# Kernel optimization log

Measured on AMD Instinct MI355X. Metric: run time of the kernel, lower is better.

The kernel has to match this reference:

```python
import jax, jax.numpy as jnp
import numpy as np

GROUP = 16  # FP4 quantization group size along the K (channel) axis
FP4_MAX = 6.0  # max magnitude representable in e2m1


def _round_e2m1(v):
    """Round to nearest value on the signed e2m1 grid {0,.5,1,1.5,2,3,4,6}."""
    s = jnp.sign(v)
    a = jnp.clip(jnp.abs(v), 0.0, FP4_MAX)
    q = jnp.where(a < 0.25, 0.0,
        jnp.where(a < 0.75, 0.5,
        jnp.where(a < 1.25, 1.0,
        jnp.where(a < 1.75, 1.5,
        jnp.where(a < 2.5, 2.0,
        jnp.where(a < 3.5, 3.0,
        jnp.where(a < 5.0, 4.0, 6.0)))))))
    return s * q


def fake_quant_fp4(x):
    """NVFP4-style fake quantization: per-16 group fp8_e4m3 scale + e2m1 values.

    x: [..., K] with K % 16 == 0. Returns dequantized tensor, same shape/dtype.
    """
    shp = x.shape
    g = x.reshape(shp[:-1] + (shp[-1] // GROUP, GROUP))
    amax = jnp.max(jnp.abs(g), axis=-1, keepdims=True)
    # scale stored as fp8_e4m3 (matches oscales dtype float8_e4m3fn in source)
    scale = (amax / FP4_MAX).astype(jnp.float8_e4m3fn).astype(x.dtype)
    safe = jnp.where(scale > 0, scale, jnp.ones_like(scale))
    q = _round_e2m1(g / safe)
    dq = jnp.where(scale > 0, q * scale, jnp.zeros_like(q))
    return dq.reshape(shp)


def setup_inputs() -> dict:
    key = jax.random.key(0)
    k1, k2, k3 = jax.random.split(key, 3)
    M, K, N = 8192, 4096, 4096
    x = jax.random.normal(k1, (M, K), dtype=jnp.float32)
    weight = jax.random.normal(k2, (N, K), dtype=jnp.float32) * 0.02
    bias = jax.random.normal(k3, (N,), dtype=jnp.float32) * 0.01
    return {"x": x, "weight": weight, "bias": bias}


def reference(x, weight, bias):
    # quantize_input: per-group FP4 fake-quant of activations (smooth == ones)
    xq = fake_quant_fp4(x)
    # __init__ quantizes weight_pad with the same kernel -> qweight/wscales
    wq = fake_quant_fp4(weight)
    # gemm_w4a4 with inline dequant + bias add
    out = jnp.einsum("mk,nk->mn", xq, wq) + bias
    return out
```

## Files before the change

### kernel.cpp

```cpp
#include <hip/hip_runtime.h>
#include <cstdint>


typedef __attribute__((ext_vector_type(8))) __bf16 bf16x8;
typedef __attribute__((ext_vector_type(4))) float f32x4;

typedef __attribute__((address_space(1))) void gvoid;
typedef __attribute__((address_space(3))) void lvoid;

__device__ __forceinline__ float fp8_e4m3_rt(float x) {
    if (x < 0.015625f) {
        return __builtin_rintf(x * 512.0f) * (1.0f / 512.0f);
    }
    unsigned u = __float_as_uint(x);
    unsigned lsb = (u >> 20) & 1u;
    u = (u + 0x7FFFFu + lsb) & ~0xFFFFFu;
    return __uint_as_float(u);
}

__device__ __forceinline__ float round_e2m1(float v) {
    float a = fabsf(v);
    a = fminf(a, 6.0f);
    float q = a < 0.25f ? 0.0f :
              a < 0.75f ? 0.5f :
              a < 1.25f ? 1.0f :
              a < 1.75f ? 1.5f :
              a < 2.5f  ? 2.0f :
              a < 3.5f  ? 3.0f :
              a < 5.0f  ? 4.0f : 6.0f;
    return copysignf(q, v);
}

__global__ __launch_bounds__(256) void quant_fp4(const float* __restrict__ in,
                                                 uint16_t* __restrict__ out,
                                                 int nquads) {
    int i = blockIdx.x * 256 + threadIdx.x;
    if (i >= nquads) return;
    float4 v = ((const float4*)in)[i];
    float a = fmaxf(fmaxf(fabsf(v.x), fabsf(v.y)), fmaxf(fabsf(v.z), fabsf(v.w)));
    a = fmaxf(a, __shfl_xor(a, 1));
    a = fmaxf(a, __shfl_xor(a, 2));
    float scale = fp8_e4m3_rt(a / 6.0f);
    float safe = scale > 0.0f ? scale : 1.0f;
    float vals[4] = {v.x, v.y, v.z, v.w};
    unsigned r[4];
    #pragma unroll
    for (int e = 0; e < 4; ++e) {
        float q = round_e2m1(vals[e] / safe);
        float dq = scale > 0.0f ? q * scale : 0.0f;
        r[e] = __float_as_uint(dq) >> 16;
    }
    uint2 o;
    o.x = r[0] | (r[1] << 16);
    o.y = r[2] | (r[3] << 16);
    ((uint2*)out)[i] = o;
}

#define BM 256
#define BN 256
#define BK 64
#define THREADS 512

__device__ __forceinline__ void barfence() {
    asm volatile("" ::: "memory");
    __builtin_amdgcn_s_barrier();
    asm volatile("" ::: "memory");
}

#define STG_A(bb, i, kk)                                                     \
    __builtin_amdgcn_global_load_lds((gvoid*)(Aq + (size_t)offA[i] + (kk)),  \
        (lvoid*)&lds[bb][0][ldsU + (i) * 4096], 16, 0, 0)
#define STG_B(bb, i, kk)                                                     \
    __builtin_amdgcn_global_load_lds((gvoid*)(Bq + (size_t)offB[i] + (kk)),  \
        (lvoid*)&lds[bb][1][ldsU + (i) * 4096], 16, 0, 0)

#define MFMA16(AH, BH, MH, NH)                                               \
    _Pragma("unroll")                                                        \
    for (int fi = 0; fi < 4; ++fi) {                                         \
        _Pragma("unroll")                                                    \
        for (int fj = 0; fj < 2; ++fj) {                                     \
            f32x4 c = acc[(MH) * 4 + fi][(NH) * 2 + fj];                     \
            c = __builtin_amdgcn_mfma_f32_16x16x32_bf16(AH[fi][0], BH[fj][0], c, 0, 0, 0); \
            c = __builtin_amdgcn_mfma_f32_16x16x32_bf16(AH[fi][1], BH[fj][1], c, 0, 0, 0); \
            acc[(MH) * 4 + fi][(NH) * 2 + fj] = c;                           \
        }                                                                    \
    }

__global__ __launch_bounds__(THREADS, 2)
void gemm_w4a4(const uint16_t* __restrict__ Aq, const uint16_t* __restrict__ Bq,
               const float* __restrict__ bias, float* __restrict__ C,
               int M, int N, int K) {
    __shared__ __align__(16) uint16_t lds[2][2][BM * BK];

    const int tid  = threadIdx.x;
    const int wave = tid >> 6;
    const int lane = tid & 63;
    const int wm   = wave >> 2;
    const int wn   = wave & 3;
    const int l15  = lane & 15;
    const int l7   = lane & 7;
    const int hi8  = (lane >> 4) << 3;
    const int hi4  = (lane >> 4) << 2;
    const int kx0  = hi8 ^ (l7 << 3);
    const int kx1  = (32 + hi8) ^ (l7 << 3);
    const int aBase = ((wm << 7) + l15) << 6;
    const int bBase = ((wn << 6) + l15) << 6;
    const int ldsU  = wave << 9;

    const int ntm = M >> 8, ntn = N >> 8, nwg = ntm * ntn;
    const int bid = blockIdx.x;
    const int q8 = nwg >> 3, r8 = nwg & 7;
    const int xcd = bid & 7;
    const int wgid = (xcd < r8 ? xcd * (q8 + 1) : r8 * (q8 + 1) + (xcd - r8) * q8)
                     + (bid >> 3);
    const int mBase = (wgid % ntm) << 8;
    const int nBase = (wgid / ntm) << 8;
    (void)ntn;

    uint32_t offA[4], offB[4];
    #pragma unroll
    for (int i = 0; i < 4; ++i) {
        const int c   = i * THREADS + tid;
        const int row = c >> 3;
        const int kc  = ((c & 7) ^ (row & 7)) << 3;
        offA[i] = (uint32_t)(mBase + row) * (uint32_t)K + (uint32_t)kc;
        offB[i] = (uint32_t)(nBase + row) * (uint32_t)K + (uint32_t)kc;
    }

    const int nt = K / BK;

    #pragma unroll
    for (int i = 0; i < 4; ++i) STG_A(0, i, 0);
    #pragma unroll
    for (int i = 0; i < 4; ++i) STG_B(0, i, 0);
    if (nt > 1) {
        #pragma unroll
        for (int i = 0; i < 4; ++i) STG_A(1, i, BK);
        #pragma unroll
        for (int i = 0; i < 4; ++i) STG_B(1, i, BK);
    }

    f32x4 acc[8][4] = {};

    for (int tk = 0; tk < nt; ++tk) {
        const int bb = tk & 1;
        const uint16_t* lA = &lds[bb][0][0];
        const uint16_t* lB = &lds[bb][1][0];
        const int kk = (tk + 2) * BK;
        const bool pf = (tk + 2) < nt;

        if (tk + 1 < nt) { asm volatile("s_waitcnt vmcnt(8)" ::: "memory"); }
        else             { asm volatile("s_waitcnt vmcnt(0)" ::: "memory"); }
        __builtin_amdgcn_s_barrier();
        asm volatile("" ::: "memory");

        bf16x8 a[4][2], b0[2][2], b1[2][2];

        #pragma unroll
        for (int fi = 0; fi < 4; ++fi) {
            a[fi][0] = *(const bf16x8*)&lA[aBase + fi * 1024 + kx0];
            a[fi][1] = *(const bf16x8*)&lA[aBase + fi * 1024 + kx1];
        }
        #pragma unroll
        for (int fj = 0; fj < 2; ++fj) {
            b0[fj][0] = *(const bf16x8*)&lB[bBase + fj * 1024 + kx0];
            b0[fj][1] = *(const bf16x8*)&lB[bBase + fj * 1024 + kx1];
        }
        barfence();
        __builtin_amdgcn_s_setprio(1);
        MFMA16(a, b0, 0, 0);
        __builtin_amdgcn_s_setprio(0);
        barfence();

        #pragma unroll
        for (int fj = 0; fj < 2; ++fj) {
            b1[fj][0] = *(const bf16x8*)&lB[bBase + 2048 + fj * 1024 + kx0];
            b1[fj][1] = *(const bf16x8*)&lB[bBase + 2048 + fj * 1024 + kx1];
        }
        if (pf) { STG_A(bb, 0, kk); STG_A(bb, 2, kk); }
        barfence();
        __builtin_amdgcn_s_setprio(1);
        MFMA16(a, b1, 0, 1);
        __builtin_amdgcn_s_setprio(0);
        barfence();

        #pragma unroll
        for (int fi = 0; fi < 4; ++fi) {
            a[fi][0] = *(const bf16x8*)&lA[aBase + 4096 + fi * 1024 + kx0];
            a[fi][1] = *(const bf16x8*)&lA[aBase + 4096 + fi * 1024 + kx1];
        }
        if (pf) { STG_B(bb, 0, kk); STG_B(bb, 1, kk); }
        barfence();
        __builtin_amdgcn_s_setprio(1);
        MFMA16(a, b1, 1, 1);
        __builtin_amdgcn_s_setprio(0);
        barfence();

        if (pf) { STG_A(bb, 1, kk); STG_A(bb, 3, kk);
                  STG_B(bb, 2, kk); STG_B(bb, 3, kk); }
        barfence();
        __builtin_amdgcn_s_setprio(1);
        MFMA16(a, b0, 1, 0);
        __builtin_amdgcn_s_setprio(0);
    }

    #pragma unroll
    for (int fj = 0; fj < 4; ++fj) {
        const int col = nBase + (wn << 6) + fj * 16 + l15;
        const float bj = bias[col];
        #pragma unroll
        for (int fi = 0; fi < 8; ++fi) {
            const int row0 = mBase + (wm << 7) + fi * 16 + hi4;
            #pragma unroll
            for (int rr = 0; rr < 4; ++rr)
                C[(size_t)(row0 + rr) * N + col] = acc[fi][fj][rr] + bj;
        }
    }
}

extern "C" void kernel_launch(void* const* d_in, const int* in_sizes, int n_in,
                              void* d_out, int out_size, void* d_ws, size_t ws_size,
                              hipStream_t stream) {
    const float* x    = (const float*)d_in[0];
    const float* w    = (const float*)d_in[1];
    const float* bias = (const float*)d_in[2];
    float* out = (float*)d_out;

    const int N = in_sizes[2];
    const int K = in_sizes[1] / N;
    const int M = in_sizes[0] / K;

    uint16_t* xq = (uint16_t*)d_ws;
    uint16_t* wq = xq + (size_t)M * K;

    const int xquads = (M * K) / 4;
    const int wquads = (N * K) / 4;
    quant_fp4<<<(xquads + 255) / 256, 256, 0, stream>>>(x, xq, xquads);
    quant_fp4<<<(wquads + 255) / 256, 256, 0, stream>>>(w, wq, wquads);

    const int nwg = (M >> 8) * (N >> 8);
    gemm_w4a4<<<nwg, THREADS, 0, stream>>>(xq, wq, bias, out, M, N, K);
}
```

Measured before the change: 498.3 us.

## Switch GEMM to 32x32x16 MFMA, simplify pipeline, fuse quant kernels

The GEMM's inner loop now uses 32x32x16 bf16 MFMA with 16-float accumulators, which reduces the number of LDS fragment reads per flop. It software-pipelines LDS reads across the four k-substeps and replaces the interleaved barrier schedule with a simple double buffer: prefetch the next tile, wait, then compute. The two quantization launches are merged into one kernel, each thread handles two quads, and the division-based e2m1 rounding is replaced with scaled FMA comparisons. The simpler prefetch only keeps one tile in flight, so global latency may be less well hidden. The FMA threshold trick may also change rounding at boundary values.

```diff
diff --git a/kernel.cpp b/kernel.cpp
--- a/kernel.cpp
+++ b/kernel.cpp
@@ -3,7 +3,7 @@
 
 
 typedef __attribute__((ext_vector_type(8))) __bf16 bf16x8;
-typedef __attribute__((ext_vector_type(4))) float f32x4;
+typedef __attribute__((ext_vector_type(16))) float f32x16;
 
 typedef __attribute__((address_space(1))) void gvoid;
 typedef __attribute__((address_space(3))) void lvoid;
@@ -18,54 +18,63 @@
     return __uint_as_float(u);
 }
 
-__device__ __forceinline__ float round_e2m1(float v) {
-    float a = fabsf(v);
-    a = fminf(a, 6.0f);
-    float q = a < 0.25f ? 0.0f :
-              a < 0.75f ? 0.5f :
-              a < 1.25f ? 1.0f :
-              a < 1.75f ? 1.5f :
-              a < 2.5f  ? 2.0f :
-              a < 3.5f  ? 3.0f :
-              a < 5.0f  ? 4.0f : 6.0f;
-    return copysignf(q, v);
-}
-
-__global__ __launch_bounds__(256) void quant_fp4(const float* __restrict__ in,
-                                                 uint16_t* __restrict__ out,
-                                                 int nquads) {
-    int i = blockIdx.x * 256 + threadIdx.x;
-    if (i >= nquads) return;
-    float4 v = ((const float4*)in)[i];
-    float a = fmaxf(fmaxf(fabsf(v.x), fabsf(v.y)), fmaxf(fabsf(v.z), fabsf(v.w)));
+__device__ __forceinline__ uint2 quant_quad(float4 v) {
+    float ax = fabsf(v.x), ay = fabsf(v.y), az = fabsf(v.z), aw = fabsf(v.w);
+    float a = fmaxf(fmaxf(ax, ay), fmaxf(az, aw));
     a = fmaxf(a, __shfl_xor(a, 1));
     a = fmaxf(a, __shfl_xor(a, 2));
     float scale = fp8_e4m3_rt(a / 6.0f);
-    float safe = scale > 0.0f ? scale : 1.0f;
-    float vals[4] = {v.x, v.y, v.z, v.w};
+    float sN = -scale;
+    float n0 = sN * 0x1p-27f;
+    float n1 = sN * 0x1p-25f;
+    float n2 = sN * 0x1p-24f;
+    float n4 = sN * 0x1p-23f;
+    float n6 = sN * 0x1p-22f;
+    float e[4] = {v.x, v.y, v.z, v.w};
     unsigned r[4];
     #pragma unroll
-    for (int e = 0; e < 4; ++e) {
-        float q = round_e2m1(vals[e] / safe);
-        float dq = scale > 0.0f ? q * scale : 0.0f;
-        r[e] = __float_as_uint(dq) >> 16;
+    for (int i = 0; i < 4; ++i) {
+        float av = fabsf(e[i]);
+        float q =
+            fmaf(sN, 0.25f, av) < n0 ? 0.0f :
+            fmaf(sN, 0.75f, av) < n1 ? 0.5f :
+            fmaf(sN, 1.25f, av) < n2 ? 1.0f :
+            fmaf(sN, 1.75f, av) < n2 ? 1.5f :
+            fmaf(sN, 2.5f,  av) < n4 ? 2.0f :
+            fmaf(sN, 3.5f,  av) < n4 ? 3.0f :
+            fmaf(sN, 5.0f,  av) < n6 ? 4.0f : 6.0f;
+        float dq = q * scale;
+        r[i] = (__float_as_uint(dq) | (__float_as_uint(e[i]) & 0x80000000u)) >> 16;
     }
     uint2 o;
     o.x = r[0] | (r[1] << 16);
     o.y = r[2] | (r[3] << 16);
-    ((uint2*)out)[i] = o;
+    return o;
+}
+
+__global__ __launch_bounds__(256)
+void quant_fp4_fused(const float* __restrict__ x, const float* __restrict__ w,
+                     uint16_t* __restrict__ out, int xquads, int totquads) {
+    const int half = totquads >> 1;
+    const int t0 = blockIdx.x * 256 + threadIdx.x;
+    uint2* o2 = (uint2*)out;
+    if (t0 < half) {
+        const float4* s0 = (t0 < xquads) ? ((const float4*)x) + t0
+                                         : ((const float4*)w) + (t0 - xquads);
+        o2[t0] = quant_quad(*s0);
+    }
+    const int q1 = t0 + half;
+    if (q1 < totquads) {
+        const float4* s1 = (q1 < xquads) ? ((const float4*)x) + q1
+                                         : ((const float4*)w) + (q1 - xquads);
+        o2[q1] = quant_quad(*s1);
+    }
 }
 
 #define BM 256
 #define BN 256
 #define BK 64
 #define THREADS 512
-
-__device__ __forceinline__ void barfence() {
-    asm volatile("" ::: "memory");
-    __builtin_amdgcn_s_barrier();
-    asm volatile("" ::: "memory");
-}
 
 #define STG_A(bb, i, kk)                                                     \
     __builtin_amdgcn_global_load_lds((gvoid*)(Aq + (size_t)offA[i] + (kk)),  \
@@ -74,18 +83,6 @@
     __builtin_amdgcn_global_load_lds((gvoid*)(Bq + (size_t)offB[i] + (kk)),  \
         (lvoid*)&lds[bb][1][ldsU + (i) * 4096], 16, 0, 0)
 
-#define MFMA16(AH, BH, MH, NH)                                               \
-    _Pragma("unroll")                                                        \
-    for (int fi = 0; fi < 4; ++fi) {                                         \
-        _Pragma("unroll")                                                    \
-        for (int fj = 0; fj < 2; ++fj) {                                     \
-            f32x4 c = acc[(MH) * 4 + fi][(NH) * 2 + fj];                     \
-            c = __builtin_amdgcn_mfma_f32_16x16x32_bf16(AH[fi][0], BH[fj][0], c, 0, 0, 0); \
-            c = __builtin_amdgcn_mfma_f32_16x16x32_bf16(AH[fi][1], BH[fj][1], c, 0, 0, 0); \
-            acc[(MH) * 4 + fi][(NH) * 2 + fj] = c;                           \
-        }                                                                    \
-    }
-
 __global__ __launch_bounds__(THREADS, 2)
 void gemm_w4a4(const uint16_t* __restrict__ Aq, const uint16_t* __restrict__ Bq,
                const float* __restrict__ bias, float* __restrict__ C,
@@ -97,15 +94,17 @@
     const int lane = tid & 63;
     const int wm   = wave >> 2;
     const int wn   = wave & 3;
-    const int l15  = lane & 15;
-    const int l7   = lane & 7;
-    const int hi8  = (lane >> 4) << 3;
-    const int hi4  = (lane >> 4) << 2;
-    const int kx0  = hi8 ^ (l7 << 3);
-    const int kx1  = (32 + hi8) ^ (l7 << 3);
-    const int aBase = ((wm << 7) + l15) << 6;
-    const int bBase = ((wn << 6) + l15) << 6;
-    const int ldsU  = wave << 9;
+    const int l31  = lane & 31;
+    const int hi8  = (lane >> 5) << 3;
+    const int rsw  = (lane & 7) << 3;
+
+    int kx[4];
+    #pragma unroll
+    for (int ks = 0; ks < 4; ++ks) kx[ks] = (ks * 16 + hi8) ^ rsw;
+
+    const int aRow = ((wm << 7) + l31) << 6;
+    const int bRow = ((wn << 6) + l31) << 6;
+    const int ldsU = wave << 9;
 
     const int ntm = M >> 8, ntn = N >> 8, nwg = ntm * ntn;
     const int bid = blockIdx.x;
@@ -133,87 +132,78 @@
     for (int i = 0; i < 4; ++i) STG_A(0, i, 0);
     #pragma unroll
     for (int i = 0; i < 4; ++i) STG_B(0, i, 0);
-    if (nt > 1) {
-        #pragma unroll
-        for (int i = 0; i < 4; ++i) STG_A(1, i, BK);
-        #pragma unroll
-        for (int i = 0; i < 4; ++i) STG_B(1, i, BK);
-    }
-
-    f32x4 acc[8][4] = {};
+
+    f32x16 acc[4][2] = {};
 
     for (int tk = 0; tk < nt; ++tk) {
         const int bb = tk & 1;
         const uint16_t* lA = &lds[bb][0][0];
         const uint16_t* lB = &lds[bb][1][0];
-        const int kk = (tk + 2) * BK;
-        const bool pf = (tk + 2) < nt;
-
-        if (tk + 1 < nt) { asm volatile("s_waitcnt vmcnt(8)" ::: "memory"); }
-        else             { asm volatile("s_waitcnt vmcnt(0)" ::: "memory"); }
+
+        asm volatile("" ::: "memory");
         __builtin_amdgcn_s_barrier();
         asm volatile("" ::: "memory");
 
-        bf16x8 a[4][2], b0[2][2], b1[2][2];
-
-        #pragma unroll
-        for (int fi = 0; fi < 4; ++fi) {
-            a[fi][0] = *(const bf16x8*)&lA[aBase + fi * 1024 + kx0];
-            a[fi][1] = *(const bf16x8*)&lA[aBase + fi * 1024 + kx1];
+        if (tk + 1 < nt) {
+            const int kk = (tk + 1) * BK;
+            #pragma unroll
+            for (int i = 0; i < 4; ++i) STG_A(bb ^ 1, i, kk);
+            #pragma unroll
+            for (int i = 0; i < 4; ++i) STG_B(bb ^ 1, i, kk);
+            asm volatile("s_waitcnt vmcnt(8)" ::: "memory");
+        } else {
+            asm volatile("s_waitcnt vmcnt(0)" ::: "memory");
         }
-        #pragma unroll
-        for (int fj = 0; fj < 2; ++fj) {
-            b0[fj][0] = *(const bf16x8*)&lB[bBase + fj * 1024 + kx0];
-            b0[fj][1] = *(const bf16x8*)&lB[bBase + fj * 1024 + kx1];
+        __builtin_amdgcn_s_barrier();
+        asm volatile("" ::: "memory");
+
+        bf16x8 aC[4], bC[2], aN[4], bN[2];
+        #pragma unroll
+        for (int mi = 0; mi < 4; ++mi)
+            aC[mi] = *(const bf16x8*)&lA[aRow + mi * 2048 + kx[0]];
+        #pragma unroll
+        for (int ni = 0; ni < 2; ++ni)
+            bC[ni] = *(const bf16x8*)&lB[bRow + ni * 2048 + kx[0]];
+
+        #pragma unroll
+        for (int ks = 0; ks < 4; ++ks) {
+            if (ks < 3) {
+                #pragma unroll
+                for (int mi = 0; mi < 4; ++mi)
+                    aN[mi] = *(const bf16x8*)&lA[aRow + mi * 2048 + kx[ks + 1]];
+                #pragma unroll
+                for (int ni = 0; ni < 2; ++ni)
+                    bN[ni] = *(const bf16x8*)&lB[bRow + ni * 2048 + kx[ks + 1]];
+            }
+            __builtin_amdgcn_s_setprio(1);
+            #pragma unroll
+            for (int mi = 0; mi < 4; ++mi)
+                #pragma unroll
+                for (int ni = 0; ni < 2; ++ni)
+                    acc[mi][ni] = __builtin_amdgcn_mfma_f32_32x32x16_bf16(
+                        aC[mi], bC[ni], acc[mi][ni], 0, 0, 0);
+            __builtin_amdgcn_s_setprio(0);
+            if (ks < 3) {
+                #pragma unroll
+                for (int mi = 0; mi < 4; ++mi) aC[mi] = aN[mi];
+                #pragma unroll
+                for (int ni = 0; ni < 2; ++ni) bC[ni] = bN[ni];
+            }
         }
-        barfence();
-        __builtin_amdgcn_s_setprio(1);
-        MFMA16(a, b0, 0, 0);
-        __builtin_amdgcn_s_setprio(0);
-        barfence();
-
-        #pragma unroll
-        for (int fj = 0; fj < 2; ++fj) {
-            b1[fj][0] = *(const bf16x8*)&lB[bBase + 2048 + fj * 1024 + kx0];
-            b1[fj][1] = *(const bf16x8*)&lB[bBase + 2048 + fj * 1024 + kx1];
-        }
-        if (pf) { STG_A(bb, 0, kk); STG_A(bb, 2, kk); }
-        barfence();
-        __builtin_amdgcn_s_setprio(1);
-        MFMA16(a, b1, 0, 1);
-        __builtin_amdgcn_s_setprio(0);
-        barfence();
-
-        #pragma unroll
-        for (int fi = 0; fi < 4; ++fi) {
-            a[fi][0] = *(const bf16x8*)&lA[aBase + 4096 + fi * 1024 + kx0];
-            a[fi][1] = *(const bf16x8*)&lA[aBase + 4096 + fi * 1024 + kx1];
-        }
-        if (pf) { STG_B(bb, 0, kk); STG_B(bb, 1, kk); }
-        barfence();
-        __builtin_amdgcn_s_setprio(1);
-        MFMA16(a, b1, 1, 1);
-        __builtin_amdgcn_s_setprio(0);
-        barfence();
-
-        if (pf) { STG_A(bb, 1, kk); STG_A(bb, 3, kk);
-                  STG_B(bb, 2, kk); STG_B(bb, 3, kk); }
-        barfence();
-        __builtin_amdgcn_s_setprio(1);
-        MFMA16(a, b0, 1, 0);
-        __builtin_amdgcn_s_setprio(0);
-    }
-
-    #pragma unroll
-    for (int fj = 0; fj < 4; ++fj) {
-        const int col = nBase + (wn << 6) + fj * 16 + l15;
+    }
+
+    #pragma unroll
+    for (int ni = 0; ni < 2; ++ni) {
+        const int col = nBase + (wn << 6) + ni * 32 + l31;
         const float bj = bias[col];
         #pragma unroll
-        for (int fi = 0; fi < 8; ++fi) {
-            const int row0 = mBase + (wm << 7) + fi * 16 + hi4;
-            #pragma unroll
-            for (int rr = 0; rr < 4; ++rr)
-                C[(size_t)(row0 + rr) * N + col] = acc[fi][fj][rr] + bj;
+        for (int mi = 0; mi < 4; ++mi) {
+            const int rowb = mBase + (wm << 7) + mi * 32 + ((lane >> 5) << 2);
+            #pragma unroll
+            for (int r = 0; r < 16; ++r) {
+                const int row = rowb + (r & 3) + ((r >> 2) << 3);
+                C[(size_t)row * N + col] = acc[mi][ni][r] + bj;
+            }
         }
     }
 }
@@ -232,11 +222,12 @@
 
     uint16_t* xq = (uint16_t*)d_ws;
     uint16_t* wq = xq + (size_t)M * K;
+    (void)wq;
 
     const int xquads = (M * K) / 4;
-    const int wquads = (N * K) / 4;
-    quant_fp4<<<(xquads + 255) / 256, 256, 0, stream>>>(x, xq, xquads);
-    quant_fp4<<<(wquads + 255) / 256, 256, 0, stream>>>(w, wq, wquads);
+    const int totquads = xquads + (N * K) / 4;
+    const int half = totquads / 2;
+    quant_fp4_fused<<<(half + 255) / 256, 256, 0, stream>>>(x, w, xq, xquads, totquads);
 
     const int nwg = (M >> 8) * (N >> 8);
     gemm_w4a4<<<nwg, THREADS, 0, stream>>>(xq, wq, bias, out, M, N, K);
```

Result: slower. 520.8 us (+4.5%).
